# Kernel tuning notes

Measured on AMD Instinct MI355X. Metric: run time of the kernel, lower is better.

Reference implementation:

```python
import jax, jax.numpy as jnp
import numpy as np

N_CLASSES = 6
EPS = 1e-12


def setup_inputs() -> dict:
    key = jax.random.key(0)
    k1, k2 = jax.random.split(key)
    N, D = 8192, 512
    latent = jax.random.normal(k1, (N, D), dtype=jnp.float32)
    # All samples are 'source' (domain == 0); this is the only consistent reading
    # of the original code (class indices are computed over the full label array).
    domain = jnp.zeros((N,), dtype=jnp.int64)
    label = jax.random.randint(k2, (N,), 0, N_CLASSES, dtype=jnp.int64)
    return {"latent": latent, "domain": domain, "label": label}


def _cosine_dist(x, y, eps=EPS):
    # cosine_dist of the original: normalize rows (norm clamped at eps),
    # Gram matrix, then abs(1 - sim) clamped at eps.
    xn = x / jnp.maximum(jnp.linalg.norm(x, axis=1, keepdims=True), eps)
    yn = y / jnp.maximum(jnp.linalg.norm(y, axis=1, keepdims=True), eps)
    sim = xn @ yn.T
    return jnp.maximum(jnp.abs(1.0 - sim), eps)


def reference(latent, domain, label):
    # domain is all zeros -> features = latent (see setup_inputs note).
    feats = latent
    N = feats.shape[0]

    # Full pairwise cosine distance [N, N] (computed once instead of per-class loops).
    D = _cosine_dist(feats, feats)

    # One-hot class membership [N, C].
    onehot = (label[:, None] == jnp.arange(N_CLASSES)[None, :]).astype(feats.dtype)
    cnt = onehot.sum(axis=0)  # [C]

    # Per-class intra-class distance sum: sum_{i,j in c} D[i, j].
    intra_sum = jnp.einsum("nc,nc->c", onehot, D @ onehot)  # [C]
    dists_class = intra_sum / (cnt * cnt - cnt)  # mean over off-diag pairs (diag is eps-clamped like original)

    # Class centroids, then F.normalize (L2, eps-clamped denominator).
    com = (onehot.T @ feats) / cnt[:, None]  # [C, D]
    com = com / jnp.maximum(jnp.linalg.norm(com, axis=1, keepdims=True), EPS)

    Dc = _cosine_dist(com, com)  # [C, C]
    mean_inter = Dc.sum() / (N_CLASSES * N_CLASSES - N_CLASSES)

    return jnp.mean(dists_class / mean_inter)
```

## Files before the change

kernel.cpp:

```cpp
#include <hip/hip_runtime.h>

#define DIMS 512
#define NCLS 6
#define EPSF 1e-12f

#define NBLK 256
#define NTHR 512
#define NWAVE 8
#define RPW 4
#define LANE_PAD 17
#define RED_W (64 * LANE_PAD)
#define PART_STRIDE 6160
#define ACCN 6156
#define FBLK 97

__device__ float g_part[NBLK * PART_STRIDE];
__device__ float g_accv[ACCN];
__device__ unsigned int g_ctr;

__global__ __launch_bounds__(NTHR, 2) void stage1(const float* __restrict__ x,
                                                  const int* __restrict__ label,
                                                  int N) {
    __shared__ float red[NWAVE * RED_W];
    __shared__ float dc[NWAVE][12];
    const int tid  = threadIdx.x;
    const int lane = tid & 63;
    const int wave = tid >> 6;
    const int gw   = blockIdx.x * NWAVE + wave;
    const int base = gw * RPW;

    float accS[NCLS][8], accT[NCLS][8], accD[NCLS], accC[NCLS];
#pragma unroll
    for (int c = 0; c < NCLS; ++c) {
        accD[c] = 0.0f; accC[c] = 0.0f;
#pragma unroll
        for (int k = 0; k < 8; ++k) { accS[c][k] = 0.0f; accT[c][k] = 0.0f; }
    }

    const float4* xf = (const float4*)x;
    float4 A[RPW], B[RPW];
    int labs[RPW];
#pragma unroll
    for (int r = 0; r < RPW; ++r) {
        const int row = (base + r < N) ? base + r : N - 1;
        A[r] = xf[row * 128 + lane];
        B[r] = xf[row * 128 + 64 + lane];
        labs[r] = label[row];
    }

    float sum[RPW];
#pragma unroll
    for (int r = 0; r < RPW; ++r)
        sum[r] = A[r].x * A[r].x + A[r].y * A[r].y + A[r].z * A[r].z + A[r].w * A[r].w
               + B[r].x * B[r].x + B[r].y * B[r].y + B[r].z * B[r].z + B[r].w * B[r].w;
#pragma unroll
    for (int off = 32; off >= 1; off >>= 1) {
#pragma unroll
        for (int r = 0; r < RPW; ++r) sum[r] += __shfl_xor(sum[r], off, 64);
    }

#pragma unroll
    for (int r = 0; r < RPW; ++r) {
        if (base + r >= N) break;
        const float inv = 1.0f / fmaxf(sqrtf(sum[r]), EPSF);
        const float nsq = sum[r] * inv * inv;
        const float4 a = A[r], b = B[r];
        const int lab = __builtin_amdgcn_readfirstlane(labs[r]);

#define UPD(c) do { \
        accS[c][0] += inv * a.x; accS[c][1] += inv * a.y; \
        accS[c][2] += inv * a.z; accS[c][3] += inv * a.w; \
        accS[c][4] += inv * b.x; accS[c][5] += inv * b.y; \
        accS[c][6] += inv * b.z; accS[c][7] += inv * b.w; \
        accT[c][0] += a.x; accT[c][1] += a.y; accT[c][2] += a.z; accT[c][3] += a.w; \
        accT[c][4] += b.x; accT[c][5] += b.y; accT[c][6] += b.z; accT[c][7] += b.w; \
        accD[c] += nsq; accC[c] += 1.0f; } while (0)

        switch (lab) {
            case 0: UPD(0); break;
            case 1: UPD(1); break;
            case 2: UPD(2); break;
            case 3: UPD(3); break;
            case 4: UPD(4); break;
            default: UPD(5); break;
        }
#undef UPD
    }

    if (lane == 0) {
#pragma unroll
        for (int c = 0; c < NCLS; ++c) { dc[wave][c] = accD[c]; dc[wave][6 + c] = accC[c]; }
    }
    float* dst = g_part + blockIdx.x * PART_STRIDE;
    float* wp  = &red[wave * RED_W + lane * LANE_PAD];
#pragma unroll
    for (int c = 0; c < NCLS; ++c) {
#pragma unroll
        for (int k = 0; k < 8; ++k) { wp[k] = accS[c][k]; wp[8 + k] = accT[c][k]; }
        __syncthreads();
#pragma unroll
        for (int half = 0; half < 2; ++half) {
            const int e = tid + half * NTHR;
            const int l = e >> 4, k = e & 15;
            float s = 0.0f;
#pragma unroll
            for (int w = 0; w < NWAVE; ++w) s += red[w * RED_W + l * LANE_PAD + k];
            dst[c * 1024 + e] = s;
        }
        __syncthreads();
    }
    if (tid < 12) {
        float s = 0.0f;
#pragma unroll
        for (int w = 0; w < NWAVE; ++w) s += dc[w][tid];
        dst[6144 + tid] = s;
    }
}

__global__ __launch_bounds__(256) void finish(float* __restrict__ out) {
    __shared__ float r2[4][72];
    __shared__ float res[48];
    __shared__ unsigned int sh_t;
    const int tid = threadIdx.x;
    const int q   = tid >> 6;
    const int l   = tid & 63;
    const int col = blockIdx.x * 64 + l;

    float s0 = 0.0f, s1 = 0.0f, s2 = 0.0f, s3 = 0.0f;
    if (col < ACCN) {
        const float* p = g_part + (size_t)(q * 64) * PART_STRIDE + col;
#pragma unroll 4
        for (int b = 0; b < 64; b += 4) {
            s0 += p[(b + 0) * PART_STRIDE];
            s1 += p[(b + 1) * PART_STRIDE];
            s2 += p[(b + 2) * PART_STRIDE];
            s3 += p[(b + 3) * PART_STRIDE];
        }
    }
    r2[q][l] = (s0 + s1) + (s2 + s3);
    __syncthreads();
    if (tid < 64) {
        const int c2 = blockIdx.x * 64 + tid;
        if (c2 < ACCN) g_accv[c2] = (r2[0][tid] + r2[1][tid]) + (r2[2][tid] + r2[3][tid]);
    }
    __syncthreads();

    if (tid == 0)
        sh_t = __hip_atomic_fetch_add(&g_ctr, 1u, __ATOMIC_ACQ_REL,
                                      __HIP_MEMORY_SCOPE_AGENT);
    __syncthreads();
    if (sh_t != (unsigned)(FBLK - 1)) return;

    const int lane = tid & 63;
    const int wave = tid >> 6;
    for (int t = wave; t < 42; t += 4) {
        float s = 0.0f;
        if (t < 6) {
            const float* p = &g_accv[t * 1024 + lane * 16];
#pragma unroll
            for (int k = 0; k < 8; ++k) s += p[k] * p[k];
        } else {
            const int pr = t - 6;
            const float* p1 = &g_accv[(pr / 6) * 1024 + lane * 16 + 8];
            const float* p2 = &g_accv[(pr % 6) * 1024 + lane * 16 + 8];
#pragma unroll
            for (int k = 0; k < 8; ++k) s += p1[k] * p2[k];
        }
#pragma unroll
        for (int off = 32; off >= 1; off >>= 1) s += __shfl_xor(s, off, 64);
        if (lane == 0) res[t] = s;
    }
    __syncthreads();

    if (tid == 0) {
        float cnt[NCLS], sd[NCLS];
        for (int c = 0; c < NCLS; ++c) {
            sd[c]  = g_accv[6144 + c];
            cnt[c] = g_accv[6150 + c];
        }
        float dsum = 0.0f;
        for (int c = 0; c < NCLS; ++c) {
            const float n2    = cnt[c] * cnt[c] - cnt[c];
            const float intra = n2 - res[c] + sd[c] + cnt[c] * EPSF;
            dsum += intra / n2;
        }
        float nrm[NCLS];
        for (int c = 0; c < NCLS; ++c)
            nrm[c] = fmaxf(sqrtf(res[6 + c * 6 + c]) / cnt[c], EPSF);
        float dcsum = 0.0f;
        for (int c1 = 0; c1 < NCLS; ++c1)
            for (int c2 = 0; c2 < NCLS; ++c2) {
                const float sim = (res[6 + c1 * 6 + c2] / (cnt[c1] * cnt[c2]))
                                / (nrm[c1] * nrm[c2]);
                dcsum += fmaxf(fabsf(1.0f - sim), EPSF);
            }
        const float mean_inter = dcsum / (float)(NCLS * NCLS - NCLS);
        out[0] = (dsum / (float)NCLS) / mean_inter;

        __hip_atomic_store(&g_ctr, 0u, __ATOMIC_RELAXED, __HIP_MEMORY_SCOPE_AGENT);
    }
}

extern "C" void kernel_launch(void* const* d_in, const int* in_sizes, int n_in,
                              void* d_out, int out_size, void* d_ws, size_t ws_size,
                              hipStream_t stream) {
    const float* latent = (const float*)d_in[0];
    const int*   label  = (const int*)d_in[2];
    const int N = in_sizes[0] / DIMS;

    stage1<<<NBLK, NTHR, 0, stream>>>(latent, label, N);
    finish<<<FBLK, 256, 0, stream>>>((float*)d_out);
}
```

Measured before the change: 31.97 us.

## Fuse stage1 and finish into one kernel with grid-wide counter barrier

Merges the two kernels into one launch. After writing partials, each block takes a ticket from an atomic counter. The last 97 blocks to arrive spin until all 256 blocks have checked in, then perform the column reduction with 8 waves. A second counter picks the final block to compute the scalar result. This removes a kernel launch and the inter-kernel gap, but relies on all 256 blocks being co-resident for the spin-wait and adds a spin barrier.

```diff
diff --git a/kernel.cpp b/kernel.cpp
--- a/kernel.cpp
+++ b/kernel.cpp
@@ -12,17 +12,22 @@
 #define RED_W (64 * LANE_PAD)
 #define PART_STRIDE 6160
 #define ACCN 6156
-#define FBLK 97
+#define NWORK 97
 
 __device__ float g_part[NBLK * PART_STRIDE];
 __device__ float g_accv[ACCN];
-__device__ unsigned int g_ctr;
-
-__global__ __launch_bounds__(NTHR, 2) void stage1(const float* __restrict__ x,
-                                                  const int* __restrict__ label,
-                                                  int N) {
+__device__ unsigned int g_ctr1;
+__device__ unsigned int g_ctr2;
+
+__global__ __launch_bounds__(NTHR, 2) void fused(const float* __restrict__ x,
+                                                 const int* __restrict__ label,
+                                                 int N, float* __restrict__ out) {
     __shared__ float red[NWAVE * RED_W];
     __shared__ float dc[NWAVE][12];
+    __shared__ float r2[8][72];
+    __shared__ float res[48];
+    __shared__ unsigned int sh_t;
+
     const int tid  = threadIdx.x;
     const int lane = tid & 63;
     const int wave = tid >> 6;
@@ -115,45 +120,53 @@
         for (int w = 0; w < NWAVE; ++w) s += dc[w][tid];
         dst[6144 + tid] = s;
     }
-}
-
-__global__ __launch_bounds__(256) void finish(float* __restrict__ out) {
-    __shared__ float r2[4][72];
-    __shared__ float res[48];
-    __shared__ unsigned int sh_t;
-    const int tid = threadIdx.x;
-    const int q   = tid >> 6;
-    const int l   = tid & 63;
-    const int col = blockIdx.x * 64 + l;
-
+    __syncthreads();
+
+    if (tid == 0)
+        sh_t = __hip_atomic_fetch_add(&g_ctr1, 1u, __ATOMIC_ACQ_REL,
+                                      __HIP_MEMORY_SCOPE_AGENT);
+    __syncthreads();
+    const unsigned ticket = sh_t;
+    if (ticket < (unsigned)(NBLK - NWORK)) return;
+
+    if (tid == 0) {
+        while (__hip_atomic_load(&g_ctr1, __ATOMIC_ACQUIRE,
+                                 __HIP_MEMORY_SCOPE_AGENT) < (unsigned)NBLK)
+            __builtin_amdgcn_s_sleep(8);
+    }
+    __syncthreads();
+
+    const int w    = (int)ticket - (NBLK - NWORK);
+    const int q    = tid >> 6;
+    const int col  = w * 64 + lane;
     float s0 = 0.0f, s1 = 0.0f, s2 = 0.0f, s3 = 0.0f;
     if (col < ACCN) {
-        const float* p = g_part + (size_t)(q * 64) * PART_STRIDE + col;
-#pragma unroll 4
-        for (int b = 0; b < 64; b += 4) {
+        const float* p = g_part + (size_t)(q * 32) * PART_STRIDE + col;
+#pragma unroll
+        for (int b = 0; b < 32; b += 4) {
             s0 += p[(b + 0) * PART_STRIDE];
             s1 += p[(b + 1) * PART_STRIDE];
             s2 += p[(b + 2) * PART_STRIDE];
             s3 += p[(b + 3) * PART_STRIDE];
         }
     }
-    r2[q][l] = (s0 + s1) + (s2 + s3);
+    r2[q][lane] = (s0 + s1) + (s2 + s3);
     __syncthreads();
     if (tid < 64) {
-        const int c2 = blockIdx.x * 64 + tid;
-        if (c2 < ACCN) g_accv[c2] = (r2[0][tid] + r2[1][tid]) + (r2[2][tid] + r2[3][tid]);
+        const int c2 = w * 64 + tid;
+        if (c2 < ACCN)
+            g_accv[c2] = ((r2[0][tid] + r2[1][tid]) + (r2[2][tid] + r2[3][tid]))
+                       + ((r2[4][tid] + r2[5][tid]) + (r2[6][tid] + r2[7][tid]));
     }
     __syncthreads();
 
     if (tid == 0)
-        sh_t = __hip_atomic_fetch_add(&g_ctr, 1u, __ATOMIC_ACQ_REL,
+        sh_t = __hip_atomic_fetch_add(&g_ctr2, 1u, __ATOMIC_ACQ_REL,
                                       __HIP_MEMORY_SCOPE_AGENT);
     __syncthreads();
-    if (sh_t != (unsigned)(FBLK - 1)) return;
-
-    const int lane = tid & 63;
-    const int wave = tid >> 6;
-    for (int t = wave; t < 42; t += 4) {
+    if (sh_t != (unsigned)(NWORK - 1)) return;
+
+    for (int t = wave; t < 42; t += NWAVE) {
         float s = 0.0f;
         if (t < 6) {
             const float* p = &g_accv[t * 1024 + lane * 16];
@@ -197,7 +210,8 @@
         const float mean_inter = dcsum / (float)(NCLS * NCLS - NCLS);
         out[0] = (dsum / (float)NCLS) / mean_inter;
 
-        __hip_atomic_store(&g_ctr, 0u, __ATOMIC_RELAXED, __HIP_MEMORY_SCOPE_AGENT);
+        __hip_atomic_store(&g_ctr1, 0u, __ATOMIC_RELAXED, __HIP_MEMORY_SCOPE_AGENT);
+        __hip_atomic_store(&g_ctr2, 0u, __ATOMIC_RELAXED, __HIP_MEMORY_SCOPE_AGENT);
     }
 }
 
@@ -208,6 +222,5 @@
     const int*   label  = (const int*)d_in[2];
     const int N = in_sizes[0] / DIMS;
 
-    stage1<<<NBLK, NTHR, 0, stream>>>(latent, label, N);
-    finish<<<FBLK, 256, 0, stream>>>((float*)d_out);
+    fused<<<NBLK, NTHR, 0, stream>>>(latent, label, N, (float*)d_out);
 }
```

Result: slower. 38.39 us (+20.1%).

## Double stage1 grid and split partial reduction into multi-kernel tree

Applied to the files above, without the earlier changes.

Stage1 now launches twice as many blocks with half the rows per wave and a higher occupancy hint. The single finish kernel, which used an atomic last-block pattern, is replaced by three kernels: a 2D chunked partial reduction, a final column reduction, and a one-block epilogue. The goal is more parallelism in both the streaming and reduction phases. In exchange the partial buffer doubles in size and two extra kernel launches are added, each with its own launch latency.

```diff
diff --git a/kernel.cpp b/kernel.cpp
--- a/kernel.cpp
+++ b/kernel.cpp
@@ -4,21 +4,22 @@
 #define NCLS 6
 #define EPSF 1e-12f
 
-#define NBLK 256
+#define NBLK 512
 #define NTHR 512
 #define NWAVE 8
-#define RPW 4
+#define RPW 2
 #define LANE_PAD 17
 #define RED_W (64 * LANE_PAD)
 #define PART_STRIDE 6160
 #define ACCN 6156
-#define FBLK 97
+#define ROWCHUNK 16
+#define NSLICE (NBLK / ROWCHUNK)
 
 __device__ float g_part[NBLK * PART_STRIDE];
+__device__ float g_part2[NSLICE * PART_STRIDE];
 __device__ float g_accv[ACCN];
-__device__ unsigned int g_ctr;
-
-__global__ __launch_bounds__(NTHR, 2) void stage1(const float* __restrict__ x,
+
+__global__ __launch_bounds__(NTHR, 4) void stage1(const float* __restrict__ x,
                                                   const int* __restrict__ label,
                                                   int N) {
     __shared__ float red[NWAVE * RED_W];
@@ -117,43 +118,42 @@
     }
 }
 
-__global__ __launch_bounds__(256) void finish(float* __restrict__ out) {
-    __shared__ float r2[4][72];
+__global__ __launch_bounds__(256) void stage2a() {
+    const int j = blockIdx.x * 256 + threadIdx.x;
+    if (j >= ACCN) return;
+    const int b0 = blockIdx.y * ROWCHUNK;
+    float s0 = 0.0f, s1 = 0.0f, s2 = 0.0f, s3 = 0.0f;
+#pragma unroll
+    for (int b = 0; b < ROWCHUNK; b += 4) {
+        s0 += g_part[(b0 + b    ) * PART_STRIDE + j];
+        s1 += g_part[(b0 + b + 1) * PART_STRIDE + j];
+        s2 += g_part[(b0 + b + 2) * PART_STRIDE + j];
+        s3 += g_part[(b0 + b + 3) * PART_STRIDE + j];
+    }
+    g_part2[blockIdx.y * PART_STRIDE + j] = (s0 + s1) + (s2 + s3);
+}
+
+__global__ __launch_bounds__(256) void stage2b() {
+    const int j = blockIdx.x * 256 + threadIdx.x;
+    if (j >= ACCN) return;
+    float s0 = 0.0f, s1 = 0.0f, s2 = 0.0f, s3 = 0.0f;
+#pragma unroll
+    for (int y = 0; y < NSLICE; y += 4) {
+        s0 += g_part2[(y    ) * PART_STRIDE + j];
+        s1 += g_part2[(y + 1) * PART_STRIDE + j];
+        s2 += g_part2[(y + 2) * PART_STRIDE + j];
+        s3 += g_part2[(y + 3) * PART_STRIDE + j];
+    }
+    g_accv[j] = (s0 + s1) + (s2 + s3);
+}
+
+__global__ __launch_bounds__(512) void stage3(float* __restrict__ out) {
     __shared__ float res[48];
-    __shared__ unsigned int sh_t;
-    const int tid = threadIdx.x;
-    const int q   = tid >> 6;
-    const int l   = tid & 63;
-    const int col = blockIdx.x * 64 + l;
-
-    float s0 = 0.0f, s1 = 0.0f, s2 = 0.0f, s3 = 0.0f;
-    if (col < ACCN) {
-        const float* p = g_part + (size_t)(q * 64) * PART_STRIDE + col;
-#pragma unroll 4
-        for (int b = 0; b < 64; b += 4) {
-            s0 += p[(b + 0) * PART_STRIDE];
-            s1 += p[(b + 1) * PART_STRIDE];
-            s2 += p[(b + 2) * PART_STRIDE];
-            s3 += p[(b + 3) * PART_STRIDE];
-        }
-    }
-    r2[q][l] = (s0 + s1) + (s2 + s3);
-    __syncthreads();
-    if (tid < 64) {
-        const int c2 = blockIdx.x * 64 + tid;
-        if (c2 < ACCN) g_accv[c2] = (r2[0][tid] + r2[1][tid]) + (r2[2][tid] + r2[3][tid]);
-    }
-    __syncthreads();
-
-    if (tid == 0)
-        sh_t = __hip_atomic_fetch_add(&g_ctr, 1u, __ATOMIC_ACQ_REL,
-                                      __HIP_MEMORY_SCOPE_AGENT);
-    __syncthreads();
-    if (sh_t != (unsigned)(FBLK - 1)) return;
-
+    const int tid  = threadIdx.x;
     const int lane = tid & 63;
     const int wave = tid >> 6;
-    for (int t = wave; t < 42; t += 4) {
+
+    for (int t = wave; t < 42; t += 8) {
         float s = 0.0f;
         if (t < 6) {
             const float* p = &g_accv[t * 1024 + lane * 16];
@@ -196,8 +196,6 @@
             }
         const float mean_inter = dcsum / (float)(NCLS * NCLS - NCLS);
         out[0] = (dsum / (float)NCLS) / mean_inter;
-
-        __hip_atomic_store(&g_ctr, 0u, __ATOMIC_RELAXED, __HIP_MEMORY_SCOPE_AGENT);
     }
 }
 
@@ -209,5 +207,8 @@
     const int N = in_sizes[0] / DIMS;
 
     stage1<<<NBLK, NTHR, 0, stream>>>(latent, label, N);
-    finish<<<FBLK, 256, 0, stream>>>((float*)d_out);
-}
+    dim3 g2a((ACCN + 255) / 256, NSLICE);
+    stage2a<<<g2a, 256, 0, stream>>>();
+    stage2b<<<(ACCN + 255) / 256, 256, 0, stream>>>();
+    stage3<<<1, 512, 0, stream>>>((float*)d_out);
+}
```

Result: slower. 53.52 us (+67.4%).

## Use branchless masked class accumulation and widen finish reduction grid

Applied to the files above, without the earlier changes.

The per-row class update switches from a switch statement to a branchless masked FMA over all six classes. Rows are now loaded one at a time in a runtime loop instead of four batched loads. The finish kernel now covers 32 columns per block with 8 chunks of 32 partials, doubling the block count for more parallel reduction. The masked update does six times the FMAs per row, and the unbatched loads reduce memory-level parallelism, in exchange for removing divergent-looking branches and register pressure.

```diff
diff --git a/kernel.cpp b/kernel.cpp
--- a/kernel.cpp
+++ b/kernel.cpp
@@ -7,27 +7,27 @@
 #define NBLK 256
 #define NTHR 512
 #define NWAVE 8
-#define RPW 4
 #define LANE_PAD 17
 #define RED_W (64 * LANE_PAD)
 #define PART_STRIDE 6160
 #define ACCN 6156
-#define FBLK 97
+#define NFIN 193
 
 __device__ float g_part[NBLK * PART_STRIDE];
 __device__ float g_accv[ACCN];
 __device__ unsigned int g_ctr;
 
-__global__ __launch_bounds__(NTHR, 2) void stage1(const float* __restrict__ x,
-                                                  const int* __restrict__ label,
-                                                  int N) {
+__global__ __launch_bounds__(NTHR) void moments(const float* __restrict__ x,
+                                                const int* __restrict__ label,
+                                                int N) {
     __shared__ float red[NWAVE * RED_W];
     __shared__ float dc[NWAVE][12];
     const int tid  = threadIdx.x;
     const int lane = tid & 63;
     const int wave = tid >> 6;
     const int gw   = blockIdx.x * NWAVE + wave;
-    const int base = gw * RPW;
+    const int nwaves = NBLK * NWAVE;
+    const int rpw = (N + nwaves - 1) / nwaves;
 
     float accS[NCLS][8], accT[NCLS][8], accD[NCLS], accC[NCLS];
 #pragma unroll
@@ -38,53 +38,34 @@
     }
 
     const float4* xf = (const float4*)x;
-    float4 A[RPW], B[RPW];
-    int labs[RPW];
+    for (int rr = 0; rr < rpw; ++rr) {
+        const int row = gw * rpw + rr;
+        if (row >= N) break;
+        const float4 a = xf[row * 128 + lane];
+        const float4 b = xf[row * 128 + 64 + lane];
+        float s = a.x * a.x + a.y * a.y + a.z * a.z + a.w * a.w
+                + b.x * b.x + b.y * b.y + b.z * b.z + b.w * b.w;
 #pragma unroll
-    for (int r = 0; r < RPW; ++r) {
-        const int row = (base + r < N) ? base + r : N - 1;
-        A[r] = xf[row * 128 + lane];
-        B[r] = xf[row * 128 + 64 + lane];
-        labs[r] = label[row];
-    }
-
-    float sum[RPW];
+        for (int off = 32; off >= 1; off >>= 1) s += __shfl_xor(s, off, 64);
+        const float nrm = fmaxf(sqrtf(s), EPSF);
+        const float inv = 1.0f / nrm;
+        const float nsq = s * inv * inv;
+        const int lab = label[row];
 #pragma unroll
-    for (int r = 0; r < RPW; ++r)
-        sum[r] = A[r].x * A[r].x + A[r].y * A[r].y + A[r].z * A[r].z + A[r].w * A[r].w
-               + B[r].x * B[r].x + B[r].y * B[r].y + B[r].z * B[r].z + B[r].w * B[r].w;
-#pragma unroll
-    for (int off = 32; off >= 1; off >>= 1) {
-#pragma unroll
-        for (int r = 0; r < RPW; ++r) sum[r] += __shfl_xor(sum[r], off, 64);
-    }
-
-#pragma unroll
-    for (int r = 0; r < RPW; ++r) {
-        if (base + r >= N) break;
-        const float inv = 1.0f / fmaxf(sqrtf(sum[r]), EPSF);
-        const float nsq = sum[r] * inv * inv;
-        const float4 a = A[r], b = B[r];
-        const int lab = __builtin_amdgcn_readfirstlane(labs[r]);
-
-#define UPD(c) do { \
-        accS[c][0] += inv * a.x; accS[c][1] += inv * a.y; \
-        accS[c][2] += inv * a.z; accS[c][3] += inv * a.w; \
-        accS[c][4] += inv * b.x; accS[c][5] += inv * b.y; \
-        accS[c][6] += inv * b.z; accS[c][7] += inv * b.w; \
-        accT[c][0] += a.x; accT[c][1] += a.y; accT[c][2] += a.z; accT[c][3] += a.w; \
-        accT[c][4] += b.x; accT[c][5] += b.y; accT[c][6] += b.z; accT[c][7] += b.w; \
-        accD[c] += nsq; accC[c] += 1.0f; } while (0)
-
-        switch (lab) {
-            case 0: UPD(0); break;
-            case 1: UPD(1); break;
-            case 2: UPD(2); break;
-            case 3: UPD(3); break;
-            case 4: UPD(4); break;
-            default: UPD(5); break;
+        for (int c = 0; c < NCLS; ++c) {
+            const float m  = (lab == c) ? 1.0f : 0.0f;
+            const float mi = m * inv;
+            accS[c][0] += mi * a.x; accS[c][1] += mi * a.y;
+            accS[c][2] += mi * a.z; accS[c][3] += mi * a.w;
+            accS[c][4] += mi * b.x; accS[c][5] += mi * b.y;
+            accS[c][6] += mi * b.z; accS[c][7] += mi * b.w;
+            accT[c][0] += m * a.x;  accT[c][1] += m * a.y;
+            accT[c][2] += m * a.z;  accT[c][3] += m * a.w;
+            accT[c][4] += m * b.x;  accT[c][5] += m * b.y;
+            accT[c][6] += m * b.z;  accT[c][7] += m * b.w;
+            accD[c] += m * nsq;
+            accC[c] += m;
         }
-#undef UPD
     }
 
     if (lane == 0) {
@@ -118,30 +99,32 @@
 }
 
 __global__ __launch_bounds__(256) void finish(float* __restrict__ out) {
-    __shared__ float r2[4][72];
+    __shared__ float r2[8][36];
     __shared__ float res[48];
     __shared__ unsigned int sh_t;
-    const int tid = threadIdx.x;
-    const int q   = tid >> 6;
-    const int l   = tid & 63;
-    const int col = blockIdx.x * 64 + l;
+    const int tid   = threadIdx.x;
+    const int ci    = tid & 31;
+    const int chunk = tid >> 5;
+    const int col   = blockIdx.x * 32 + ci;
 
     float s0 = 0.0f, s1 = 0.0f, s2 = 0.0f, s3 = 0.0f;
     if (col < ACCN) {
-        const float* p = g_part + (size_t)(q * 64) * PART_STRIDE + col;
-#pragma unroll 4
-        for (int b = 0; b < 64; b += 4) {
+        const float* p = g_part + (size_t)(chunk * 32) * PART_STRIDE + col;
+#pragma unroll
+        for (int b = 0; b < 32; b += 4) {
             s0 += p[(b + 0) * PART_STRIDE];
             s1 += p[(b + 1) * PART_STRIDE];
             s2 += p[(b + 2) * PART_STRIDE];
             s3 += p[(b + 3) * PART_STRIDE];
         }
     }
-    r2[q][l] = (s0 + s1) + (s2 + s3);
+    r2[chunk][ci] = (s0 + s1) + (s2 + s3);
     __syncthreads();
-    if (tid < 64) {
-        const int c2 = blockIdx.x * 64 + tid;
-        if (c2 < ACCN) g_accv[c2] = (r2[0][tid] + r2[1][tid]) + (r2[2][tid] + r2[3][tid]);
+    if (tid < 32) {
+        const int c2 = blockIdx.x * 32 + tid;
+        if (c2 < ACCN)
+            g_accv[c2] = ((r2[0][tid] + r2[1][tid]) + (r2[2][tid] + r2[3][tid]))
+                       + ((r2[4][tid] + r2[5][tid]) + (r2[6][tid] + r2[7][tid]));
     }
     __syncthreads();
 
@@ -149,7 +132,7 @@
         sh_t = __hip_atomic_fetch_add(&g_ctr, 1u, __ATOMIC_ACQ_REL,
                                       __HIP_MEMORY_SCOPE_AGENT);
     __syncthreads();
-    if (sh_t != (unsigned)(FBLK - 1)) return;
+    if (sh_t != (unsigned)(NFIN - 1)) return;
 
     const int lane = tid & 63;
     const int wave = tid >> 6;
@@ -208,6 +191,6 @@
     const int*   label  = (const int*)d_in[2];
     const int N = in_sizes[0] / DIMS;
 
-    stage1<<<NBLK, NTHR, 0, stream>>>(latent, label, N);
-    finish<<<FBLK, 256, 0, stream>>>((float*)d_out);
+    moments<<<NBLK, NTHR, 0, stream>>>(latent, label, N);
+    finish<<<NFIN, 256, 0, stream>>>((float*)d_out);
 }
```

Measured after the change: 32.26 us. Within noise of the previous version (+0.9%).
